# Kernel optimization log

Hardware: AMD Instinct MI355X
Metric: run time of the kernel (lower is better)

The kernel has to match this reference:

```python
import jax, jax.numpy as jnp
import numpy as np


def setup_inputs() -> dict:
    key = jax.random.key(0)
    k1, k2 = jax.random.split(key)
    x = jax.random.normal(k1, (32, 256, 56, 56), dtype=jnp.float32)
    # Conv2d(2 -> 1, kernel 7x7, bias=False): weight [out_c=1, in_c=2, 7, 7]
    w_conv = jax.random.normal(k2, (1, 2, 7, 7), dtype=jnp.float32) * 0.1
    return {"x": x, "w_conv": w_conv}


def reference(x, w_conv):
    # channel-wise average and max pooling -> [B, 2, H, W]
    avgout = jnp.mean(x, axis=1, keepdims=True)
    maxout = jnp.max(x, axis=1, keepdims=True)
    x1 = jnp.concatenate([avgout, maxout], axis=1)
    # 7x7 conv, padding=3 (SAME), NCHW / OIHW
    x1 = jax.lax.conv_general_dilated(
        x1, w_conv,
        window_strides=(1, 1),
        padding=((3, 3), (3, 3)),
        dimension_numbers=("NCHW", "OIHW", "NCHW"),
    )
    gate = jax.nn.sigmoid(x1)  # [B, 1, H, W]
    return x * gate
```

## Files before the change

### kernel.cpp

```cpp
#include <hip/hip_runtime.h>
#include <math.h>

#define B_    32
#define C_    256
#define H_    56
#define W_    56
#define HW_   (H_ * W_)
#define BHW_  (B_ * HW_)
#define HW4_  (HW_ / 4)
#define NF4_  (BHW_ / 4)
#define GRID_ 784
#define CHUNKF4_ (NF4_ / GRID_)
#define POSPB_  (BHW_ / GRID_)

typedef float f4v __attribute__((ext_vector_type(4)));

__global__ __launch_bounds__(512, 6) void sa_reduce_kernel(
    const float* __restrict__ x, float* __restrict__ pool) {
  const int t = threadIdx.x;
  const int lane = t & 31;
  const int cgrp = t >> 5;
  const unsigned if4 = (unsigned)blockIdx.x * CHUNKF4_ + lane;
  const unsigned bimg = if4 / HW4_;
  const unsigned hw4 = if4 % HW4_;
  const f4v* __restrict__ x4 = (const f4v*)x;
  const unsigned base = (bimg * C_ + cgrp * 16) * HW4_ + hw4;

  f4v s = {0.f, 0.f, 0.f, 0.f};
  f4v m = {-INFINITY, -INFINITY, -INFINITY, -INFINITY};
#pragma unroll 8
  for (int k = 0; k < 16; ++k) {
    f4v v = x4[base + (unsigned)k * HW4_];
    s += v;
    m = (f4v){fmaxf(m.x, v.x), fmaxf(m.y, v.y),
              fmaxf(m.z, v.z), fmaxf(m.w, v.w)};
  }

  __shared__ f4v ssum[16][32];
  __shared__ f4v smax[16][32];
  ssum[cgrp][lane] = s;
  smax[cgrp][lane] = m;
  __syncthreads();

  if (t < 32) {
    f4v S = ssum[0][t];
    f4v M = smax[0][t];
#pragma unroll
    for (int g = 1; g < 16; ++g) {
      f4v sg = ssum[g][t];
      f4v mg = smax[g][t];
      S += sg;
      M = (f4v){fmaxf(M.x, mg.x), fmaxf(M.y, mg.y),
                fmaxf(M.z, mg.z), fmaxf(M.w, mg.w)};
    }
    f4v* p4 = (f4v*)pool;
    const unsigned jf4 = (unsigned)blockIdx.x * CHUNKF4_ + t;
    const unsigned bb = jf4 / HW4_;
    const unsigned hh = jf4 % HW4_;
    p4[bb * 2 * HW4_ + hh]        = S * (1.0f / (float)C_);
    p4[bb * 2 * HW4_ + HW4_ + hh] = M;
  }
}

__global__ __launch_bounds__(512, 6) void sa_conv_apply_kernel(
    const float* __restrict__ x, const float* __restrict__ pool,
    const float* __restrict__ wt, float* __restrict__ out) {
  const int t = threadIdx.x;
  __shared__ float partial[512];
  __shared__ f4v sgate4[CHUNKF4_];

  {
    const int pos = t >> 2;
    const int sub = t & 3;
    const int ic = sub & 1;
    const int khalf = sub >> 1;
    const unsigned p = (unsigned)blockIdx.x * POSPB_ + (unsigned)pos;
    const unsigned bimg_a = p / HW_;
    const unsigned hw = p % HW_;
    const int h = (int)(hw / W_);
    const int w = (int)(hw % W_);
    const float* pl = pool + ((long)bimg_a * 2 + ic) * HW_;
    const float* wr0 = wt + ic * 49;
    const int kh0 = khalf ? 4 : 0;
    const int kh1 = khalf ? 7 : 4;
    float acc = 0.f;
    for (int kh = kh0; kh < kh1; ++kh) {
      const int ih = h + kh - 3;
      if (ih < 0 || ih >= H_) continue;
      const float* row = pl + ih * W_;
      const float* wr = wr0 + kh * 7;
#pragma unroll
      for (int kw = 0; kw < 7; ++kw) {
        const int iw = w + kw - 3;
        if (iw < 0 || iw >= W_) continue;
        acc = fmaf(row[iw], wr[kw], acc);
      }
    }
    partial[t] = acc;
  }
  __syncthreads();
  if (t < POSPB_) {
    float a = partial[4 * t] + partial[4 * t + 1] +
              partial[4 * t + 2] + partial[4 * t + 3];
    ((float*)sgate4)[t] = 1.0f / (1.0f + __expf(-a));
  }
  __syncthreads();

  const int lane = t & 31;
  const int cgrp = t >> 5;
  const unsigned if4 = (unsigned)blockIdx.x * CHUNKF4_ + lane;
  const unsigned bimg = if4 / HW4_;
  const unsigned hw4 = if4 % HW4_;
  const unsigned base = (bimg * C_ + cgrp * 16) * HW4_ + hw4;
  const f4v* __restrict__ x4 = (const f4v*)x;
  f4v* __restrict__ o4 = (f4v*)out;
  const f4v g = sgate4[lane];
#pragma unroll 8
  for (int k = 0; k < 16; ++k) {
    const unsigned idx = base + (unsigned)k * HW4_;
    f4v v = x4[idx];
    __builtin_nontemporal_store(v * g, &o4[idx]);
  }
}

extern "C" void kernel_launch(void* const* d_in, const int* in_sizes, int n_in,
                              void* d_out, int out_size, void* d_ws, size_t ws_size,
                              hipStream_t stream) {
  const float* x  = (const float*)d_in[0];
  const float* wc = (const float*)d_in[1];
  float* out = (float*)d_out;
  float* pool = (float*)d_ws;

  sa_reduce_kernel<<<GRID_, 512, 0, stream>>>(x, pool);
  sa_conv_apply_kernel<<<GRID_, 512, 0, stream>>>(x, pool, wc, out);
}
```

Before: 208.4 us.

## Fuse reduce and conv-apply into one persistent kernel with a grid barrier

```diff
diff --git a/kernel.cpp b/kernel.cpp
--- a/kernel.cpp
+++ b/kernel.cpp
@@ -10,34 +10,67 @@
 #define HW4_  (HW_ / 4)
 #define NF4_  (BHW_ / 4)
 #define GRID_ 784
-#define CHUNKF4_ (NF4_ / GRID_)
-#define POSPB_  (BHW_ / GRID_)
+#define CHUNKF4_ 32
+#define POSPB_   128
+#define NXCD_ 8
+#define F4PX_ (NF4_ / NXCD_)
 
 typedef float f4v __attribute__((ext_vector_type(4)));
 
-__global__ __launch_bounds__(512, 6) void sa_reduce_kernel(
-    const float* __restrict__ x, float* __restrict__ pool) {
+__device__ unsigned g_count;
+__device__ unsigned g_release;
+
+__device__ __forceinline__ void grid_barrier(int t) {
+  __syncthreads();
+  if (t == 0) {
+    __threadfence();
+    unsigned old = atomicAdd(&g_count, 1u);
+    unsigned epoch = old / (unsigned)GRID_;
+    if (old % (unsigned)GRID_ == (unsigned)(GRID_ - 1)) {
+      atomicAdd(&g_release, 1u);
+    } else {
+      unsigned spins = 0;
+      while (__hip_atomic_load(&g_release, __ATOMIC_ACQUIRE,
+                               __HIP_MEMORY_SCOPE_AGENT) <= epoch) {
+        __builtin_amdgcn_s_sleep(16);
+        if (++spins > 4000000u) break;
+      }
+    }
+    __threadfence();
+  }
+  __syncthreads();
+}
+
+__global__ __launch_bounds__(256, 4) void sa_fused_kernel(
+    const float* __restrict__ x, const float* __restrict__ wt,
+    float* __restrict__ out, float* __restrict__ pool) {
   const int t = threadIdx.x;
+  const unsigned b = blockIdx.x;
+  const unsigned xcd = b % NXCD_;
+  const unsigned j = b / NXCD_;
+  const unsigned if4base = xcd * F4PX_ + j * CHUNKF4_;
+
   const int lane = t & 31;
   const int cgrp = t >> 5;
-  const unsigned if4 = (unsigned)blockIdx.x * CHUNKF4_ + lane;
+  const unsigned if4 = if4base + (unsigned)lane;
   const unsigned bimg = if4 / HW4_;
   const unsigned hw4 = if4 % HW4_;
   const f4v* __restrict__ x4 = (const f4v*)x;
-  const unsigned base = (bimg * C_ + cgrp * 16) * HW4_ + hw4;
+  f4v* __restrict__ o4 = (f4v*)out;
+  const unsigned base = (bimg * C_ + (unsigned)cgrp * 32u) * HW4_ + hw4;
 
   f4v s = {0.f, 0.f, 0.f, 0.f};
   f4v m = {-INFINITY, -INFINITY, -INFINITY, -INFINITY};
 #pragma unroll 8
-  for (int k = 0; k < 16; ++k) {
+  for (int k = 0; k < 32; ++k) {
     f4v v = x4[base + (unsigned)k * HW4_];
     s += v;
     m = (f4v){fmaxf(m.x, v.x), fmaxf(m.y, v.y),
               fmaxf(m.z, v.z), fmaxf(m.w, v.w)};
   }
 
-  __shared__ f4v ssum[16][32];
-  __shared__ f4v smax[16][32];
+  __shared__ f4v ssum[8][32];
+  __shared__ f4v smax[8][32];
   ssum[cgrp][lane] = s;
   smax[cgrp][lane] = m;
   __syncthreads();
@@ -46,7 +79,7 @@
     f4v S = ssum[0][t];
     f4v M = smax[0][t];
 #pragma unroll
-    for (int g = 1; g < 16; ++g) {
+    for (int g = 1; g < 8; ++g) {
       f4v sg = ssum[g][t];
       f4v mg = smax[g][t];
       S += sg;
@@ -54,37 +87,30 @@
                 fmaxf(M.z, mg.z), fmaxf(M.w, mg.w)};
     }
     f4v* p4 = (f4v*)pool;
-    const unsigned jf4 = (unsigned)blockIdx.x * CHUNKF4_ + t;
+    const unsigned jf4 = if4base + (unsigned)t;
     const unsigned bb = jf4 / HW4_;
     const unsigned hh = jf4 % HW4_;
     p4[bb * 2 * HW4_ + hh]        = S * (1.0f / (float)C_);
     p4[bb * 2 * HW4_ + HW4_ + hh] = M;
   }
-}
 
-__global__ __launch_bounds__(512, 6) void sa_conv_apply_kernel(
-    const float* __restrict__ x, const float* __restrict__ pool,
-    const float* __restrict__ wt, float* __restrict__ out) {
-  const int t = threadIdx.x;
-  __shared__ float partial[512];
+  grid_barrier(t);
+
+  __shared__ float partial[256];
   __shared__ f4v sgate4[CHUNKF4_];
-
   {
-    const int pos = t >> 2;
-    const int sub = t & 3;
-    const int ic = sub & 1;
-    const int khalf = sub >> 1;
-    const unsigned p = (unsigned)blockIdx.x * POSPB_ + (unsigned)pos;
+    const int pos = t >> 1;
+    const int ic = t & 1;
+    const unsigned p = if4base * 4u + (unsigned)pos;
     const unsigned bimg_a = p / HW_;
     const unsigned hw = p % HW_;
     const int h = (int)(hw / W_);
     const int w = (int)(hw % W_);
     const float* pl = pool + ((long)bimg_a * 2 + ic) * HW_;
     const float* wr0 = wt + ic * 49;
-    const int kh0 = khalf ? 4 : 0;
-    const int kh1 = khalf ? 7 : 4;
     float acc = 0.f;
-    for (int kh = kh0; kh < kh1; ++kh) {
+#pragma unroll
+    for (int kh = 0; kh < 7; ++kh) {
       const int ih = h + kh - 3;
       if (ih < 0 || ih >= H_) continue;
       const float* row = pl + ih * W_;
@@ -100,23 +126,14 @@
   }
   __syncthreads();
   if (t < POSPB_) {
-    float a = partial[4 * t] + partial[4 * t + 1] +
-              partial[4 * t + 2] + partial[4 * t + 3];
+    float a = partial[2 * t] + partial[2 * t + 1];
     ((float*)sgate4)[t] = 1.0f / (1.0f + __expf(-a));
   }
   __syncthreads();
 
-  const int lane = t & 31;
-  const int cgrp = t >> 5;
-  const unsigned if4 = (unsigned)blockIdx.x * CHUNKF4_ + lane;
-  const unsigned bimg = if4 / HW4_;
-  const unsigned hw4 = if4 % HW4_;
-  const unsigned base = (bimg * C_ + cgrp * 16) * HW4_ + hw4;
-  const f4v* __restrict__ x4 = (const f4v*)x;
-  f4v* __restrict__ o4 = (f4v*)out;
   const f4v g = sgate4[lane];
 #pragma unroll 8
-  for (int k = 0; k < 16; ++k) {
+  for (int k = 0; k < 32; ++k) {
     const unsigned idx = base + (unsigned)k * HW4_;
     f4v v = x4[idx];
     __builtin_nontemporal_store(v * g, &o4[idx]);
@@ -131,6 +148,5 @@
   float* out = (float*)d_out;
   float* pool = (float*)d_ws;
 
-  sa_reduce_kernel<<<GRID_, 512, 0, stream>>>(x, pool);
-  sa_conv_apply_kernel<<<GRID_, 512, 0, stream>>>(x, pool, wc, out);
+  sa_fused_kernel<<<GRID_, 256, 0, stream>>>(x, wc, out, pool);
 }
```

Measured after the change: 318.8 us. 1.53x slower.
